# Kernel tuning notes

Hardware: AMD Instinct MI355X
Metric: run time of the kernel (lower is better)

## Reference

```python
import jax, jax.numpy as jnp
import numpy as np

B, NQ, NKV, D, H = 2, 2048, 2048, 1024, 16
DH = D // H
EPS = 1e-5


def _ln(x, g, b):
    mu = jnp.mean(x, axis=-1, keepdims=True)
    var = jnp.mean(jnp.square(x - mu), axis=-1, keepdims=True)
    return (x - mu) * jax.lax.rsqrt(var + EPS) * g + b


def setup_inputs() -> dict:
    key = jax.random.key(0)
    ks = jax.random.split(key, 16)
    s = 0.02
    return {
        "X": jax.random.normal(ks[0], (B, NQ, D), jnp.float32),
        "Y": jax.random.normal(ks[1], (B, NKV, D), jnp.float32),
        "Wq": jax.random.normal(ks[2], (D, D), jnp.float32) * s,
        "bq": jnp.zeros((D,), jnp.float32),
        "Wk": jax.random.normal(ks[3], (D, D), jnp.float32) * s,
        "bk": jnp.zeros((D,), jnp.float32),
        "Wv": jax.random.normal(ks[4], (D, D), jnp.float32) * s,
        "bv": jnp.zeros((D,), jnp.float32),
        "null_k": jax.random.normal(ks[5], (1, 1, D), jnp.float32) * s,
        "g0": jnp.ones((D,), jnp.float32),
        "b0": jnp.zeros((D,), jnp.float32),
        "g0kv": jnp.ones((D,), jnp.float32),
        "b0kv": jnp.zeros((D,), jnp.float32),
        "g1": jnp.ones((D,), jnp.float32),
        "b1": jnp.zeros((D,), jnp.float32),
        "W1": jax.random.normal(ks[6], (D, 4 * D), jnp.float32) * s,
        "bf1": jnp.zeros((4 * D,), jnp.float32),
        "W2": jax.random.normal(ks[7], (4 * D, D), jnp.float32) * s,
        "bf2": jnp.zeros((D,), jnp.float32),
    }


def reference(X, Y, Wq, bq, Wk, bk, Wv, bv, null_k, g0, b0, g0kv, b0kv,
              g1, b1, W1, bf1, W2, bf2):
    # pre-layer-norm on Q-side and KV-side inputs
    Xn = _ln(X, g0, b0)
    Yn = _ln(Y, g0kv, b0kv)
    Q = Xn @ Wq + bq                       # [B, NQ, D]
    K = Yn @ Wk + bk                       # [B, NKV, D]
    V = Yn @ Wv + bv
    # null KV: learned null key, zero value appended along seq dim
    K = jnp.concatenate([K, jnp.broadcast_to(null_k, (B, 1, D))], axis=1)   # [B, NKV+1, D]
    V = jnp.concatenate([V, jnp.zeros((B, 1, D), V.dtype)], axis=1)
    # split heads (split along feature dim == reshape to (.., H, DH))
    Qh = Q.reshape(B, NQ, H, DH)
    Kh = K.reshape(B, NKV + 1, H, DH)
    Vh = V.reshape(B, NKV + 1, H, DH)
    # scores scaled by 1/sqrt(dim_KV) (NOT head dim), softmax_temp == 1.0
    A = jnp.einsum('bqhd,bkhd->bhqk', Qh, Kh) / jnp.sqrt(jnp.float32(D))
    A = jax.nn.softmax(A, axis=-1)          # [B, H, NQ, NKV+1]
    O = jnp.einsum('bhqk,bkhd->bqhd', A, Vh).reshape(B, NQ, D)
    # no head mixing (fc_mix_heads=None); residual uses identity fc_res
    Hres = O + X
    Hr = _ln(Hres, g1, b1)
    ff = jax.nn.gelu(Hr @ W1 + bf1, approximate=False) @ W2 + bf2
    return Hres + ff
```

## Files before the change

### kernel.cpp

```cpp
#include <hip/hip_runtime.h>
#include <hip/hip_bf16.h>
#include <math.h>
#include <stdint.h>

typedef __bf16 bf16x8 __attribute__((ext_vector_type(8)));
typedef __bf16 bf16x4 __attribute__((ext_vector_type(4)));
typedef float floatx4 __attribute__((ext_vector_type(4)));
typedef short shortx4 __attribute__((ext_vector_type(4)));
typedef unsigned int uint32x2 __attribute__((ext_vector_type(2)));

#define NQS   2048
#define NKVS  2048
#define NKV1  2049
#define DM    1024
#define NH    16
#define DHD   64
#define BATCH 2
#define ROWS  (BATCH * NQS)

__device__ __forceinline__ void gld_lds16(const __bf16* gp, __bf16* lp) {
    __builtin_amdgcn_global_load_lds(
        (const __attribute__((address_space(1))) uint32_t*)(uintptr_t)gp,
        (__attribute__((address_space(3))) uint32_t*)(uintptr_t)lp,
        16, 0, 0);
}

__device__ __forceinline__ float gelu_fast(float x) {
    const float u = x * x;
    const float e = __builtin_amdgcn_exp2f(x * (-2.3022077f + (-0.1029431f) * u));
    return x * __builtin_amdgcn_rcpf(1.0f + e);
}

__global__ __launch_bounds__(256) void ln2_to_bf16(
    const float* __restrict__ X, const float* __restrict__ Y,
    const float* __restrict__ g0, const float* __restrict__ b0,
    const float* __restrict__ g0kv, const float* __restrict__ b0kv,
    __bf16* __restrict__ Xn, __bf16* __restrict__ Yn)
{
    int row = blockIdx.x;
    const float *src, *gamma, *beta; __bf16* dst;
    if (row < ROWS) { src = X; gamma = g0; beta = b0; dst = Xn; }
    else { row -= ROWS; src = Y; gamma = g0kv; beta = b0kv; dst = Yn; }
    const int tid = threadIdx.x;
    const float4 v = ((const float4*)(src + (size_t)row * DM))[tid];
    float s  = v.x + v.y + v.z + v.w;
    float sq = v.x * v.x + v.y * v.y + v.z * v.z + v.w * v.w;
    for (int off = 1; off < 64; off <<= 1) {
        s  += __shfl_xor(s, off);
        sq += __shfl_xor(sq, off);
    }
    __shared__ float red[8];
    const int wave = tid >> 6, lane = tid & 63;
    if (lane == 0) { red[wave * 2] = s; red[wave * 2 + 1] = sq; }
    __syncthreads();
    s  = red[0] + red[2] + red[4] + red[6];
    sq = red[1] + red[3] + red[5] + red[7];
    const float mu  = s * (1.0f / DM);
    const float var = sq * (1.0f / DM) - mu * mu;
    const float rs  = rsqrtf(var + 1e-5f);
    const float4 gv = ((const float4*)gamma)[tid];
    const float4 bv = ((const float4*)beta)[tid];
    bf16x4 o;
    o[0] = (__bf16)((v.x - mu) * rs * gv.x + bv.x);
    o[1] = (__bf16)((v.y - mu) * rs * gv.y + bv.y);
    o[2] = (__bf16)((v.z - mu) * rs * gv.z + bv.z);
    o[3] = (__bf16)((v.w - mu) * rs * gv.w + bv.w);
    *(bf16x4*)(dst + (size_t)row * DM + tid * 4) = o;
}

__global__ __launch_bounds__(256) void resid_ln(
    const float* __restrict__ X, const __bf16* __restrict__ O,
    const float* __restrict__ gamma, const float* __restrict__ beta,
    float* __restrict__ Hres, __bf16* __restrict__ Hr)
{
    const int row = blockIdx.x;
    const int tid = threadIdx.x;
    const float4 xv = ((const float4*)(X + (size_t)row * DM))[tid];
    const bf16x4 ov = *(const bf16x4*)(O + (size_t)row * DM + tid * 4);
    float4 v;
    v.x = xv.x + (float)ov[0];
    v.y = xv.y + (float)ov[1];
    v.z = xv.z + (float)ov[2];
    v.w = xv.w + (float)ov[3];
    ((float4*)(Hres + (size_t)row * DM))[tid] = v;

    float s  = v.x + v.y + v.z + v.w;
    float sq = v.x * v.x + v.y * v.y + v.z * v.z + v.w * v.w;
    for (int off = 1; off < 64; off <<= 1) {
        s  += __shfl_xor(s, off);
        sq += __shfl_xor(sq, off);
    }
    __shared__ float red[8];
    const int wave = tid >> 6, lane = tid & 63;
    if (lane == 0) { red[wave * 2] = s; red[wave * 2 + 1] = sq; }
    __syncthreads();
    s  = red[0] + red[2] + red[4] + red[6];
    sq = red[1] + red[3] + red[5] + red[7];
    const float mu  = s * (1.0f / DM);
    const float var = sq * (1.0f / DM) - mu * mu;
    const float rs  = rsqrtf(var + 1e-5f);
    const float4 gv = ((const float4*)gamma)[tid];
    const float4 bv = ((const float4*)beta)[tid];
    bf16x4 o;
    o[0] = (__bf16)((v.x - mu) * rs * gv.x + bv.x);
    o[1] = (__bf16)((v.y - mu) * rs * gv.y + bv.y);
    o[2] = (__bf16)((v.z - mu) * rs * gv.z + bv.z);
    o[3] = (__bf16)((v.w - mu) * rs * gv.w + bv.w);
    *(bf16x4*)(Hr + (size_t)row * DM + tid * 4) = o;
}

__global__ __launch_bounds__(256) void transpose3_f32_bf16(
    const float* __restrict__ Wq, const float* __restrict__ Wk,
    const float* __restrict__ Wv, __bf16* __restrict__ WqT,
    __bf16* __restrict__ WkT, __bf16* __restrict__ WvT)
{
    __shared__ float tile[32][33];
    const int z = blockIdx.z;
    const float* in = (z == 0) ? Wq : (z == 1) ? Wk : Wv;
    __bf16* out = (z == 0) ? WqT : (z == 1) ? WkT : WvT;
    const int c0 = blockIdx.x * 32, r0 = blockIdx.y * 32;
    const int tx = threadIdx.x, ty = threadIdx.y;
#pragma unroll
    for (int i = 0; i < 4; i++)
        tile[ty + i * 8][tx] = in[(size_t)(r0 + ty + i * 8) * DM + c0 + tx];
    __syncthreads();
#pragma unroll
    for (int i = 0; i < 4; i++)
        out[(size_t)(c0 + ty + i * 8) * DM + r0 + tx] = (__bf16)tile[tx][ty + i * 8];
}

__global__ __launch_bounds__(256) void transpose_ffw(
    const float* __restrict__ W1, const float* __restrict__ W2,
    __bf16* __restrict__ W1T, __bf16* __restrict__ W2T)
{
    __shared__ float tile[32][33];
    const int z = blockIdx.z;
    const float* in; __bf16* out; int R, C, c0, r0;
    if (z == 0) { in = W1; out = W1T; R = DM; C = 4 * DM; c0 = blockIdx.x * 32; r0 = blockIdx.y * 32; }
    else        { in = W2; out = W2T; R = 4 * DM; C = DM; c0 = blockIdx.y * 32; r0 = blockIdx.x * 32; }
    const int tx = threadIdx.x, ty = threadIdx.y;
#pragma unroll
    for (int i = 0; i < 4; i++)
        tile[ty + i * 8][tx] = in[(size_t)(r0 + ty + i * 8) * C + c0 + tx];
    __syncthreads();
#pragma unroll
    for (int i = 0; i < 4; i++)
        out[(size_t)(c0 + ty + i * 8) * R + r0 + tx] = (__bf16)tile[tx][ty + i * 8];
}

__global__ __launch_bounds__(256) void fill_null(
    const float* __restrict__ null_k, __bf16* __restrict__ Kb,
    __bf16* __restrict__ Vt)
{
    const int i = blockIdx.x * 256 + threadIdx.x;
    if (i < BATCH * DM) {
        const int b = i >> 10, d = i & (DM - 1);
        Kb[((size_t)b * NKV1 + NKVS) * DM + d] = (__bf16)null_k[d];
    }
    if (i < BATCH * NH * DHD * 8) {
        const int bhd = i >> 3, kvp = i & 7;
        Vt[(size_t)bhd * 2056 + 2048 + kvp] = (__bf16)0.0f;
    }
}

template<int MODE, int ACT>
__global__ __launch_bounds__(256) void gemm_bt(
    const __bf16* __restrict__ A, const __bf16* __restrict__ Bt,
    const float* __restrict__ bias, void* __restrict__ outp,
    const float* __restrict__ resid, int M, int N, int K)
{
    __shared__ __bf16 As[128][32];
    __shared__ __bf16 Bs[128][32];
    const int tid  = threadIdx.x;
    const int lane = tid & 63, wave = tid >> 6;
    const int g = lane >> 4, c = lane & 15;
    const int m0 = blockIdx.y * 128, n0 = blockIdx.x * 128;
    const int wm = (wave >> 1) * 64, wn = (wave & 1) * 64;

    floatx4 acc[4][4] = {};

    const int srow = tid >> 2;
    const int schk = (tid & 3) * 8;
    const __bf16* Ag = A  + (size_t)(m0 + srow) * K + schk;
    const __bf16* Bg = Bt + (size_t)(n0 + srow) * K + schk;
    __bf16* lA0 = &As[srow][schk];
    __bf16* lA1 = &As[srow + 64][schk];
    __bf16* lB0 = &Bs[srow][schk];
    __bf16* lB1 = &Bs[srow + 64][schk];

    int kbeg = 0, kend = K;
    if (MODE == 4) { const int KS = K >> 2; kbeg = blockIdx.z * KS; kend = kbeg + KS; }

    for (int k0 = kbeg; k0 < kend; k0 += 32) {
        __syncthreads();
        gld_lds16(Ag + k0, lA0);
        gld_lds16(Ag + (size_t)64 * K + k0, lA1);
        gld_lds16(Bg + k0, lB0);
        gld_lds16(Bg + (size_t)64 * K + k0, lB1);
        __syncthreads();
        bf16x8 af[4], bfr[4];
#pragma unroll
        for (int i = 0; i < 4; i++) af[i]  = *(const bf16x8*)&As[wm + i * 16 + c][g * 8];
#pragma unroll
        for (int j = 0; j < 4; j++) bfr[j] = *(const bf16x8*)&Bs[wn + j * 16 + c][g * 8];
#pragma unroll
        for (int i = 0; i < 4; i++)
#pragma unroll
            for (int j = 0; j < 4; j++)
                acc[i][j] = __builtin_amdgcn_mfma_f32_16x16x32_bf16(af[i], bfr[j], acc[i][j], 0, 0, 0);
    }

    __bf16* obf = (__bf16*)outp;
    float*  of  = (float*)outp;
#pragma unroll
    for (int i = 0; i < 4; i++) {
#pragma unroll
        for (int j = 0; j < 4; j++) {
            const int row = m0 + wm + i * 16 + g * 4;
            const int col = n0 + wn + j * 16 + c;
            const float bb = (MODE == 4) ? 0.0f : bias[col];
            float xs[4];
#pragma unroll
            for (int r = 0; r < 4; r++) {
                float x = acc[i][j][r] + bb;
                if (ACT == 1) x = gelu_fast(x);
                xs[r] = x;
            }
            if (MODE == 0) {
#pragma unroll
                for (int r = 0; r < 4; r++)
                    obf[(size_t)(row + r) * N + col] = (__bf16)xs[r];
            } else if (MODE == 4) {
#pragma unroll
                for (int r = 0; r < 4; r++)
                    of[((size_t)blockIdx.z * M + row + r) * N + col] = xs[r];
            }
        }
    }
}

__global__ __launch_bounds__(256) void qkv_gemm(
    const __bf16* __restrict__ Xn, const __bf16* __restrict__ Yn,
    const __bf16* __restrict__ WqT, const __bf16* __restrict__ WkT,
    const __bf16* __restrict__ WvT,
    const float* __restrict__ bq, const float* __restrict__ bk,
    const float* __restrict__ bv,
    __bf16* __restrict__ Qbf, __bf16* __restrict__ Kbf,
    __bf16* __restrict__ Vt)
{
    __shared__ __bf16 As[128][32];
    __shared__ __bf16 Bs[128][32];
    const int z = blockIdx.z;
    const __bf16* A    = (z == 0) ? Xn  : Yn;
    const __bf16* Bt   = (z == 0) ? WqT : (z == 1) ? WkT : WvT;
    const float*  bias = (z == 0) ? bq  : (z == 1) ? bk  : bv;

    const int tid  = threadIdx.x;
    const int lane = tid & 63, wave = tid >> 6;
    const int g = lane >> 4, c = lane & 15;
    const int m0 = blockIdx.y * 128, n0 = blockIdx.x * 128;
    const int wm = (wave >> 1) * 64, wn = (wave & 1) * 64;

    floatx4 acc[4][4] = {};

    const int srow = tid >> 2;
    const int schk = (tid & 3) * 8;
    const __bf16* Ag = A  + (size_t)(m0 + srow) * DM + schk;
    const __bf16* Bg = Bt + (size_t)(n0 + srow) * DM + schk;
    __bf16* lA0 = &As[srow][schk];
    __bf16* lA1 = &As[srow + 64][schk];
    __bf16* lB0 = &Bs[srow][schk];
    __bf16* lB1 = &Bs[srow + 64][schk];

    for (int k0 = 0; k0 < DM; k0 += 32) {
        __syncthreads();
        gld_lds16(Ag + k0, lA0);
        gld_lds16(Ag + (size_t)64 * DM + k0, lA1);
        gld_lds16(Bg + k0, lB0);
        gld_lds16(Bg + (size_t)64 * DM + k0, lB1);
        __syncthreads();
        bf16x8 af[4], bfr[4];
#pragma unroll
        for (int i = 0; i < 4; i++) af[i]  = *(const bf16x8*)&As[wm + i * 16 + c][g * 8];
#pragma unroll
        for (int j = 0; j < 4; j++) bfr[j] = *(const bf16x8*)&Bs[wn + j * 16 + c][g * 8];
#pragma unroll
        for (int i = 0; i < 4; i++)
#pragma unroll
            for (int j = 0; j < 4; j++)
                acc[i][j] = __builtin_amdgcn_mfma_f32_16x16x32_bf16(af[i], bfr[j], acc[i][j], 0, 0, 0);
    }

#pragma unroll
    for (int i = 0; i < 4; i++) {
#pragma unroll
        for (int j = 0; j < 4; j++) {
            const int row = m0 + wm + i * 16 + g * 4;
            const int col = n0 + wn + j * 16 + c;
            const float bb = bias[col];
            float xs[4];
#pragma unroll
            for (int r = 0; r < 4; r++) xs[r] = acc[i][j][r] + bb;
            if (z == 0) {
#pragma unroll
                for (int r = 0; r < 4; r++)
                    Qbf[(size_t)(row + r) * DM + col] = (__bf16)xs[r];
            } else if (z == 1) {
#pragma unroll
                for (int r = 0; r < 4; r++) {
                    const int rr = row + r;
                    Kbf[(size_t)(rr + (rr >> 11)) * DM + col] = (__bf16)xs[r];
                }
            } else {
                const int b  = row >> 11;
                const int kv = row & 2047;
                const size_t base =
                    ((size_t)((b * NH + (col >> 6)) * DHD + (col & 63))) * 2056 + kv;
                bf16x4 pk;
                pk[0] = (__bf16)xs[0]; pk[1] = (__bf16)xs[1];
                pk[2] = (__bf16)xs[2]; pk[3] = (__bf16)xs[3];
                *(bf16x4*)(Vt + base) = pk;
            }
        }
    }
}

__global__ __launch_bounds__(256) void ff2_reduce(
    const float* __restrict__ part, const float* __restrict__ bias,
    const float* __restrict__ Hres, float* __restrict__ out)
{
    const size_t f4 = (size_t)blockIdx.x * 256 + threadIdx.x;
    const int c4 = (int)(f4 & (DM / 4 - 1));
    const size_t stride4 = (size_t)ROWS * DM / 4;
    float4 a = ((const float4*)part)[f4];
    const float4 p1 = ((const float4*)part)[f4 + stride4];
    const float4 p2 = ((const float4*)part)[f4 + 2 * stride4];
    const float4 p3 = ((const float4*)part)[f4 + 3 * stride4];
    const float4 b  = ((const float4*)bias)[c4];
    const float4 hr = ((const float4*)Hres)[f4];
    a.x += p1.x + p2.x + p3.x + b.x + hr.x;
    a.y += p1.y + p2.y + p3.y + b.y + hr.y;
    a.z += p1.z + p2.z + p3.z + b.z + hr.z;
    a.w += p1.w + p2.w + p3.w + b.w + hr.w;
    ((float4*)out)[f4] = a;
}

__global__ __launch_bounds__(256, 2) void attn_kernel(
    const __bf16* __restrict__ Q, const __bf16* __restrict__ Kb,
    const __bf16* __restrict__ Vt, __bf16* __restrict__ O)
{
    __shared__ __bf16 Ks[2][64][64];
    __shared__ __bf16 Vs[2][64][64];

    const int tid = threadIdx.x, lane = tid & 63, w = tid >> 6;
    const int g = lane >> 4, c = lane & 15;

    const int hw   = blockIdx.x;
    const int slot = hw >> 3;
    const int hb   = (hw & 7) | ((slot >> 4) << 3);
    const int h = hb & 15, b = hb >> 4;
    const int q0w = (slot & 15) * 128 + w * 32;

    const float QSC = 0.03125f * 1.44269504088896f;
    bf16x8 qf[2][2];
#pragma unroll
    for (int qt = 0; qt < 2; qt++) {
        const __bf16* Qbase = Q + ((size_t)(b * NQS + q0w + qt * 16 + c)) * DM + h * DHD;
        qf[qt][0] = *(const bf16x8*)(Qbase + g * 8);
        qf[qt][1] = *(const bf16x8*)(Qbase + 32 + g * 8);
#pragma unroll
        for (int e = 0; e < 8; e++) {
            qf[qt][0][e] = (__bf16)((float)qf[qt][0][e] * QSC);
            qf[qt][1][e] = (__bf16)((float)qf[qt][1][e] * QSC);
        }
    }

    floatx4 lacc[2] = {};
    floatx4 oacc[2][4] = {};

    const int srow = tid >> 3;
    const int schk = (tid & 7) ^ (srow & 7);
    const __bf16* Kg  = Kb + (size_t)b * NKV1 * DM + h * DHD + schk * 8;
    const __bf16* Vg  = Vt + ((size_t)(b * NH + h) * DHD + srow) * 2056;
    const __bf16* Vg2 = Vg + (size_t)32 * 2056;
    const int vcol0 = schk * 8;

    auto stage = [&](int p, int kv0, bool tail) {
        __bf16* kd0 = &Ks[p][0][0]  + tid * 8;
        __bf16* kd1 = &Ks[p][32][0] + tid * 8;
        __bf16* vd0 = &Vs[p][0][0]  + tid * 8;
        __bf16* vd1 = &Vs[p][32][0] + tid * 8;
        if (!tail) {
            gld_lds16(Kg + (size_t)(kv0 + srow) * DM, kd0);
            gld_lds16(Kg + (size_t)(kv0 + srow + 32) * DM, kd1);
            gld_lds16(Vg + kv0 + vcol0, vd0);
            gld_lds16(Vg2 + kv0 + vcol0, vd1);
        } else {
            const int r0 = min(kv0 + srow, NKVS);
            const int r1 = min(kv0 + srow + 32, NKVS);
            const int vc = min(kv0 + vcol0, NKVS);
            gld_lds16(Kg + (size_t)r0 * DM, kd0);
            gld_lds16(Kg + (size_t)r1 * DM, kd1);
            gld_lds16(Vg + vc, vd0);
            gld_lds16(Vg2 + vc, vd1);
        }
    };

    auto compute = [&](int p, int kv0, bool tail) {
        floatx4 s[2][4];
#pragma unroll
        for (int qt = 0; qt < 2; qt++)
#pragma unroll
            for (int kvt = 0; kvt < 4; kvt++)
#pragma unroll
                for (int r = 0; r < 4; r++) s[qt][kvt][r] = -6.0f;

        const int sw = c & 7;
        __builtin_amdgcn_s_setprio(1);
#pragma unroll
        for (int kvt = 0; kvt < 4; kvt++) {
            const bf16x8 kf0 = *(const bf16x8*)&Ks[p][kvt * 16 + c][(g ^ sw) * 8];
            const bf16x8 kf1 = *(const bf16x8*)&Ks[p][kvt * 16 + c][((4 | g) ^ sw) * 8];
#pragma unroll
            for (int qt = 0; qt < 2; qt++) {
                s[qt][kvt] = __builtin_amdgcn_mfma_f32_16x16x32_bf16(kf0, qf[qt][0], s[qt][kvt], 0, 0, 0);
                s[qt][kvt] = __builtin_amdgcn_mfma_f32_16x16x32_bf16(kf1, qf[qt][1], s[qt][kvt], 0, 0, 0);
            }
        }
        __builtin_amdgcn_s_setprio(0);

        if (tail) {
#pragma unroll
            for (int qt = 0; qt < 2; qt++)
#pragma unroll
                for (int kvt = 0; kvt < 4; kvt++)
#pragma unroll
                    for (int r = 0; r < 4; r++)
                        if (kv0 + kvt * 16 + g * 4 + r >= NKV1) s[qt][kvt][r] = -1e30f;
        }

        shortx4 pf[2][4];
#pragma unroll
        for (int qt = 0; qt < 2; qt++)
#pragma unroll
            for (int kvt = 0; kvt < 4; kvt++) {
                float p0 = __builtin_amdgcn_exp2f(s[qt][kvt][0]);
                float p1 = __builtin_amdgcn_exp2f(s[qt][kvt][1]);
                float p2 = __builtin_amdgcn_exp2f(s[qt][kvt][2]);
                float p3 = __builtin_amdgcn_exp2f(s[qt][kvt][3]);
                lacc[qt][0] += p0; lacc[qt][1] += p1;
                lacc[qt][2] += p2; lacc[qt][3] += p3;
                uint32x2 pk;
                pk[0] = (__builtin_bit_cast(unsigned int, p0) >> 16) |
                        (__builtin_bit_cast(unsigned int, p1) & 0xFFFF0000u);
                pk[1] = (__builtin_bit_cast(unsigned int, p2) >> 16) |
                        (__builtin_bit_cast(unsigned int, p3) & 0xFFFF0000u);
                pf[qt][kvt] = __builtin_bit_cast(shortx4, pk);
            }

        __builtin_amdgcn_s_setprio(1);
#pragma unroll
        for (int kvt = 0; kvt < 4; kvt++) {
            shortx4 vfr[4];
#pragma unroll
            for (int dt = 0; dt < 4; dt++) {
                const int slotp = (kvt * 2 + (g >> 1)) ^ sw;
                vfr[dt] = *(const shortx4*)&Vs[p][dt * 16 + c][slotp * 8 + (g & 1) * 4];
            }
#pragma unroll
            for (int dt = 0; dt < 4; dt++)
#pragma unroll
                for (int qt = 0; qt < 2; qt++)
                    oacc[qt][dt] = __builtin_amdgcn_mfma_f32_16x16x16bf16_1k(
                        vfr[dt], pf[qt][kvt], oacc[qt][dt], 0, 0, 0);
        }
        __builtin_amdgcn_s_setprio(0);
    };

    stage(0, 0, false);
    __syncthreads();
    for (int it = 0; it < 32; it++) {
        stage((it + 1) & 1, (it + 1) * 64, it == 31);
        compute(it & 1, it * 64, false);
        __syncthreads();
    }
    compute(0, 2048, true);

#pragma unroll
    for (int qt = 0; qt < 2; qt++) {
        float l = lacc[qt][0] + lacc[qt][1] + lacc[qt][2] + lacc[qt][3];
        l += __shfl_xor(l, 16);
        l += __shfl_xor(l, 32);
        const float inv_l = 1.0f / l;
        __bf16* Ob = O + ((size_t)(b * NQS + q0w + qt * 16 + c)) * DM + h * DHD;
#pragma unroll
        for (int dt = 0; dt < 4; dt++) {
            bf16x4 ob;
#pragma unroll
            for (int r = 0; r < 4; r++) ob[r] = (__bf16)(oacc[qt][dt][r] * inv_l);
            *(bf16x4*)(Ob + dt * 16 + g * 4) = ob;
        }
    }
}

extern "C" void kernel_launch(void* const* d_in, const int* in_sizes, int n_in,
                              void* d_out, int out_size, void* d_ws, size_t ws_size,
                              hipStream_t stream)
{
    const float* X      = (const float*)d_in[0];
    const float* Y      = (const float*)d_in[1];
    const float* Wq     = (const float*)d_in[2];
    const float* bq     = (const float*)d_in[3];
    const float* Wk     = (const float*)d_in[4];
    const float* bk     = (const float*)d_in[5];
    const float* Wv     = (const float*)d_in[6];
    const float* bv     = (const float*)d_in[7];
    const float* null_k = (const float*)d_in[8];
    const float* g0     = (const float*)d_in[9];
    const float* b0     = (const float*)d_in[10];
    const float* g0kv   = (const float*)d_in[11];
    const float* b0kv   = (const float*)d_in[12];
    const float* g1     = (const float*)d_in[13];
    const float* b1     = (const float*)d_in[14];
    const float* W1     = (const float*)d_in[15];
    const float* bf1    = (const float*)d_in[16];
    const float* W2     = (const float*)d_in[17];
    const float* bf2    = (const float*)d_in[18];
    float* out = (float*)d_out;

    char* p = (char*)d_ws;
    __bf16* W2T  = (__bf16*)p; p += (size_t)4 * DM * DM * 2;
    float*  Hres = (float*)p;  p += (size_t)ROWS * DM * 4;
    __bf16* Gbf  = (__bf16*)p; p += (size_t)ROWS * 4 * DM * 2;
    char* scratch = p;
    __bf16* Xn   = (__bf16*)p; p += (size_t)ROWS * DM * 2;
    __bf16* Yn   = (__bf16*)p; p += (size_t)ROWS * DM * 2;
    __bf16* WqT  = (__bf16*)p; p += (size_t)DM * DM * 2;
    __bf16* WkT  = (__bf16*)p; p += (size_t)DM * DM * 2;
    __bf16* WvT  = (__bf16*)p; p += (size_t)DM * DM * 2;
    __bf16* W1T  = (__bf16*)p; p += (size_t)4 * DM * DM * 2;
    __bf16* Qbf  = (__bf16*)p; p += (size_t)ROWS * DM * 2;
    __bf16* Kbf  = (__bf16*)p; p += (size_t)BATCH * NKV1 * DM * 2;
    __bf16* Vt   = (__bf16*)p; p += (size_t)BATCH * NH * DHD * 2056 * 2;
    __bf16* Obf  = (__bf16*)p; p += (size_t)ROWS * DM * 2;
    __bf16* Hr   = (__bf16*)p; p += (size_t)ROWS * DM * 2;
    float* Part  = (float*)scratch;

    ln2_to_bf16<<<2 * ROWS, 256, 0, stream>>>(X, Y, g0, b0, g0kv, b0kv, Xn, Yn);

    transpose3_f32_bf16<<<dim3(DM / 32, DM / 32, 3), dim3(32, 8), 0, stream>>>(
        Wq, Wk, Wv, WqT, WkT, WvT);
    transpose_ffw<<<dim3(128, 32, 2), dim3(32, 8), 0, stream>>>(W1, W2, W1T, W2T);

    qkv_gemm<<<dim3(DM / 128, ROWS / 128, 3), 256, 0, stream>>>(
        Xn, Yn, WqT, WkT, WvT, bq, bk, bv, Qbf, Kbf, Vt);
    fill_null<<<64, 256, 0, stream>>>(null_k, Kbf, Vt);

    attn_kernel<<<dim3(512), 256, 0, stream>>>(Qbf, Kbf, Vt, Obf);

    resid_ln<<<ROWS, 256, 0, stream>>>(X, Obf, g1, b1, Hres, Hr);

    gemm_bt<0, 1><<<dim3(4 * DM / 128, ROWS / 128), 256, 0, stream>>>(
        Hr, W1T, bf1, (void*)Gbf, nullptr, ROWS, 4 * DM, DM);
    gemm_bt<4, 0><<<dim3(DM / 128, ROWS / 128, 4), 256, 0, stream>>>(
        Gbf, W2T, bf2, (void*)Part, nullptr, ROWS, DM, 4 * DM);
    ff2_reduce<<<ROWS * DM / 1024, 256, 0, stream>>>(Part, bf2, Hres, out);
}
```

Before: 390.1 us.

## Replace GEMMs with 256x256 tiles and four-stage async LDS pipeline

Replaces the 128x128 single-buffered GEMM kernels (QKV, FF1, FF2) with a shared 256x256-tile, 512-thread main loop. It keeps four LDS stages in flight using global_load_lds with explicit vmcnt waits, XOR-swizzles the LDS layout to avoid bank conflicts, raises wave priority around the MFMA block, and remaps block ids for L2 locality. The goal is to hide global load latency and raise MFMA utilization. In exchange it uses much more LDS (128KB per block) and fewer blocks, so occupancy drops and the tail is coarser, e.g. only 192 blocks for QKV.

```diff
diff --git a/kernel.cpp b/kernel.cpp
--- a/kernel.cpp
+++ b/kernel.cpp
@@ -163,83 +163,135 @@
     }
 }
 
-template<int MODE, int ACT>
-__global__ __launch_bounds__(256) void gemm_bt(
+__device__ __forceinline__ void g256_loop(
+    const __bf16* __restrict__ A, const __bf16* __restrict__ Bt,
+    int Kst, int kbeg, int m0, int n0,
+    __bf16* sa, __bf16* sb, floatx4 (&acc)[8][4])
+{
+    const int tid = threadIdx.x, lane = tid & 63;
+    const int g = lane >> 4, c = lane & 15;
+    const int wave = tid >> 6;
+    const int wm = wave >> 2, wn = wave & 3;
+
+    const int r = tid >> 2, j = tid & 3;
+    const int jx = (j ^ (r & 3)) * 8;
+    const __bf16* Ag = A  + (size_t)(m0 + r) * Kst + kbeg + jx;
+    const __bf16* Bg = Bt + (size_t)(n0 + r) * Kst + kbeg + jx;
+    __bf16* la = sa + tid * 8;
+    __bf16* lb = sb + tid * 8;
+
+#define G256_STAGE(ss, koff) do {                                          \
+    gld_lds16(Ag + (koff),                      la + (ss) * 8192);         \
+    gld_lds16(Ag + (size_t)128 * Kst + (koff),  la + (ss) * 8192 + 4096);  \
+    gld_lds16(Bg + (koff),                      lb + (ss) * 8192);         \
+    gld_lds16(Bg + (size_t)128 * Kst + (koff),  lb + (ss) * 8192 + 4096);  \
+} while (0)
+
+    G256_STAGE(0, 0);
+    G256_STAGE(1, 32);
+    G256_STAGE(2, 64);
+
+    const int ca = (c & 3) * 8;
+    const __bf16* ra = sa + (wm * 128 + c) * 32;
+    const __bf16* rb = sb + (wn * 64 + c) * 32;
+
+    for (int s = 0; s < 32; s++) {
+        if (s < 29) {
+            G256_STAGE((s + 3) & 3, (s + 3) * 32);
+            asm volatile("s_waitcnt vmcnt(12)" ::: "memory");
+        } else if (s == 29) {
+            asm volatile("s_waitcnt vmcnt(8)" ::: "memory");
+        } else if (s == 30) {
+            asm volatile("s_waitcnt vmcnt(4)" ::: "memory");
+        } else {
+            asm volatile("s_waitcnt vmcnt(0)" ::: "memory");
+        }
+        __builtin_amdgcn_sched_barrier(0);
+        __builtin_amdgcn_s_barrier();
+        asm volatile("" ::: "memory");
+
+        const int ss = (s & 3) * 8192;
+        bf16x8 af[8], bfr[4];
+#pragma unroll
+        for (int i = 0; i < 8; i++)
+            af[i] = *(const bf16x8*)(ra + ss + i * 512 + ((g * 8) ^ ca));
+#pragma unroll
+        for (int jj = 0; jj < 4; jj++)
+            bfr[jj] = *(const bf16x8*)(rb + ss + jj * 512 + ((g * 8) ^ ca));
+
+        __builtin_amdgcn_s_setprio(1);
+#pragma unroll
+        for (int i = 0; i < 8; i++)
+#pragma unroll
+            for (int jj = 0; jj < 4; jj++)
+                acc[i][jj] = __builtin_amdgcn_mfma_f32_16x16x32_bf16(
+                    af[i], bfr[jj], acc[i][jj], 0, 0, 0);
+        __builtin_amdgcn_s_setprio(0);
+        __builtin_amdgcn_sched_barrier(0);
+        __builtin_amdgcn_s_barrier();
+        asm volatile("" ::: "memory");
+    }
+#undef G256_STAGE
+}
+
+template<int NX>
+__device__ __forceinline__ void g256_decode(int bid, int ntot, int& m0, int& n0)
+{
+    const int cpx = ntot >> 3;
+    const int l = (bid & 7) * cpx + (bid >> 3);
+    m0 = (l / NX) * 256;
+    n0 = (l % NX) * 256;
+}
+
+template<int MODE, int ACT, int NX>
+__global__ __launch_bounds__(512, 2) void g256(
     const __bf16* __restrict__ A, const __bf16* __restrict__ Bt,
     const float* __restrict__ bias, void* __restrict__ outp,
-    const float* __restrict__ resid, int M, int N, int K)
-{
-    __shared__ __bf16 As[128][32];
-    __shared__ __bf16 Bs[128][32];
-    const int tid  = threadIdx.x;
-    const int lane = tid & 63, wave = tid >> 6;
+    int M, int N, int Kst)
+{
+    __shared__ __bf16 SA[4][256][32];
+    __shared__ __bf16 SB[4][256][32];
+    int m0, n0;
+    g256_decode<NX>(blockIdx.x, NX * (M >> 8), m0, n0);
+    const int kbeg = (MODE == 4) ? (blockIdx.z << 10) : 0;
+
+    floatx4 acc[8][4] = {};
+    g256_loop(A, Bt, Kst, kbeg, m0, n0, &SA[0][0][0], &SB[0][0][0], acc);
+
+    const int tid = threadIdx.x, lane = tid & 63, wave = tid >> 6;
     const int g = lane >> 4, c = lane & 15;
-    const int m0 = blockIdx.y * 128, n0 = blockIdx.x * 128;
-    const int wm = (wave >> 1) * 64, wn = (wave & 1) * 64;
-
-    floatx4 acc[4][4] = {};
-
-    const int srow = tid >> 2;
-    const int schk = (tid & 3) * 8;
-    const __bf16* Ag = A  + (size_t)(m0 + srow) * K + schk;
-    const __bf16* Bg = Bt + (size_t)(n0 + srow) * K + schk;
-    __bf16* lA0 = &As[srow][schk];
-    __bf16* lA1 = &As[srow + 64][schk];
-    __bf16* lB0 = &Bs[srow][schk];
-    __bf16* lB1 = &Bs[srow + 64][schk];
-
-    int kbeg = 0, kend = K;
-    if (MODE == 4) { const int KS = K >> 2; kbeg = blockIdx.z * KS; kend = kbeg + KS; }
-
-    for (int k0 = kbeg; k0 < kend; k0 += 32) {
-        __syncthreads();
-        gld_lds16(Ag + k0, lA0);
-        gld_lds16(Ag + (size_t)64 * K + k0, lA1);
-        gld_lds16(Bg + k0, lB0);
-        gld_lds16(Bg + (size_t)64 * K + k0, lB1);
-        __syncthreads();
-        bf16x8 af[4], bfr[4];
-#pragma unroll
-        for (int i = 0; i < 4; i++) af[i]  = *(const bf16x8*)&As[wm + i * 16 + c][g * 8];
-#pragma unroll
-        for (int j = 0; j < 4; j++) bfr[j] = *(const bf16x8*)&Bs[wn + j * 16 + c][g * 8];
-#pragma unroll
-        for (int i = 0; i < 4; i++)
-#pragma unroll
-            for (int j = 0; j < 4; j++)
-                acc[i][j] = __builtin_amdgcn_mfma_f32_16x16x32_bf16(af[i], bfr[j], acc[i][j], 0, 0, 0);
-    }
+    const int wm = wave >> 2, wn = wave & 3;
 
     __bf16* obf = (__bf16*)outp;
     float*  of  = (float*)outp;
 #pragma unroll
-    for (int i = 0; i < 4; i++) {
-#pragma unroll
-        for (int j = 0; j < 4; j++) {
-            const int row = m0 + wm + i * 16 + g * 4;
-            const int col = n0 + wn + j * 16 + c;
+    for (int i = 0; i < 8; i++) {
+#pragma unroll
+        for (int jj = 0; jj < 4; jj++) {
+            const int row = m0 + wm * 128 + i * 16 + g * 4;
+            const int col = n0 + wn * 64 + jj * 16 + c;
             const float bb = (MODE == 4) ? 0.0f : bias[col];
             float xs[4];
 #pragma unroll
-            for (int r = 0; r < 4; r++) {
-                float x = acc[i][j][r] + bb;
+            for (int rr = 0; rr < 4; rr++) {
+                float x = acc[i][jj][rr] + bb;
                 if (ACT == 1) x = gelu_fast(x);
-                xs[r] = x;
+                xs[rr] = x;
             }
             if (MODE == 0) {
 #pragma unroll
-                for (int r = 0; r < 4; r++)
-                    obf[(size_t)(row + r) * N + col] = (__bf16)xs[r];
+                for (int rr = 0; rr < 4; rr++)
+                    obf[(size_t)(row + rr) * N + col] = (__bf16)xs[rr];
             } else if (MODE == 4) {
 #pragma unroll
-                for (int r = 0; r < 4; r++)
-                    of[((size_t)blockIdx.z * M + row + r) * N + col] = xs[r];
+                for (int rr = 0; rr < 4; rr++)
+                    of[((size_t)blockIdx.z * M + row + rr) * N + col] = xs[rr];
             }
         }
     }
 }
 
-__global__ __launch_bounds__(256) void qkv_gemm(
+__global__ __launch_bounds__(512, 2) void g256qkv(
     const __bf16* __restrict__ Xn, const __bf16* __restrict__ Yn,
     const __bf16* __restrict__ WqT, const __bf16* __restrict__ WkT,
     const __bf16* __restrict__ WvT,
@@ -248,68 +300,42 @@
     __bf16* __restrict__ Qbf, __bf16* __restrict__ Kbf,
     __bf16* __restrict__ Vt)
 {
-    __shared__ __bf16 As[128][32];
-    __shared__ __bf16 Bs[128][32];
+    __shared__ __bf16 SA[4][256][32];
+    __shared__ __bf16 SB[4][256][32];
     const int z = blockIdx.z;
     const __bf16* A    = (z == 0) ? Xn  : Yn;
     const __bf16* Bt   = (z == 0) ? WqT : (z == 1) ? WkT : WvT;
     const float*  bias = (z == 0) ? bq  : (z == 1) ? bk  : bv;
 
-    const int tid  = threadIdx.x;
-    const int lane = tid & 63, wave = tid >> 6;
+    int m0, n0;
+    g256_decode<4>(blockIdx.x, 64, m0, n0);
+
+    floatx4 acc[8][4] = {};
+    g256_loop(A, Bt, DM, 0, m0, n0, &SA[0][0][0], &SB[0][0][0], acc);
+
+    const int tid = threadIdx.x, lane = tid & 63, wave = tid >> 6;
     const int g = lane >> 4, c = lane & 15;
-    const int m0 = blockIdx.y * 128, n0 = blockIdx.x * 128;
-    const int wm = (wave >> 1) * 64, wn = (wave & 1) * 64;
-
-    floatx4 acc[4][4] = {};
-
-    const int srow = tid >> 2;
-    const int schk = (tid & 3) * 8;
-    const __bf16* Ag = A  + (size_t)(m0 + srow) * DM + schk;
-    const __bf16* Bg = Bt + (size_t)(n0 + srow) * DM + schk;
-    __bf16* lA0 = &As[srow][schk];
-    __bf16* lA1 = &As[srow + 64][schk];
-    __bf16* lB0 = &Bs[srow][schk];
-    __bf16* lB1 = &Bs[srow + 64][schk];
-
-    for (int k0 = 0; k0 < DM; k0 += 32) {
-        __syncthreads();
-        gld_lds16(Ag + k0, lA0);
-        gld_lds16(Ag + (size_t)64 * DM + k0, lA1);
-        gld_lds16(Bg + k0, lB0);
-        gld_lds16(Bg + (size_t)64 * DM + k0, lB1);
-        __syncthreads();
-        bf16x8 af[4], bfr[4];
-#pragma unroll
-        for (int i = 0; i < 4; i++) af[i]  = *(const bf16x8*)&As[wm + i * 16 + c][g * 8];
-#pragma unroll
-        for (int j = 0; j < 4; j++) bfr[j] = *(const bf16x8*)&Bs[wn + j * 16 + c][g * 8];
-#pragma unroll
-        for (int i = 0; i < 4; i++)
-#pragma unroll
-            for (int j = 0; j < 4; j++)
-                acc[i][j] = __builtin_amdgcn_mfma_f32_16x16x32_bf16(af[i], bfr[j], acc[i][j], 0, 0, 0);
-    }
-
-#pragma unroll
-    for (int i = 0; i < 4; i++) {
-#pragma unroll
-        for (int j = 0; j < 4; j++) {
-            const int row = m0 + wm + i * 16 + g * 4;
-            const int col = n0 + wn + j * 16 + c;
+    const int wm = wave >> 2, wn = wave & 3;
+
+#pragma unroll
+    for (int i = 0; i < 8; i++) {
+#pragma unroll
+        for (int jj = 0; jj < 4; jj++) {
+            const int row = m0 + wm * 128 + i * 16 + g * 4;
+            const int col = n0 + wn * 64 + jj * 16 + c;
             const float bb = bias[col];
             float xs[4];
 #pragma unroll
-            for (int r = 0; r < 4; r++) xs[r] = acc[i][j][r] + bb;
+            for (int rr = 0; rr < 4; rr++) xs[rr] = acc[i][jj][rr] + bb;
             if (z == 0) {
 #pragma unroll
-                for (int r = 0; r < 4; r++)
-                    Qbf[(size_t)(row + r) * DM + col] = (__bf16)xs[r];
+                for (int rr = 0; rr < 4; rr++)
+                    Qbf[(size_t)(row + rr) * DM + col] = (__bf16)xs[rr];
             } else if (z == 1) {
 #pragma unroll
-                for (int r = 0; r < 4; r++) {
-                    const int rr = row + r;
-                    Kbf[(size_t)(rr + (rr >> 11)) * DM + col] = (__bf16)xs[r];
+                for (int rr = 0; rr < 4; rr++) {
+                    const int r2 = row + rr;
+                    Kbf[(size_t)(r2 + (r2 >> 11)) * DM + col] = (__bf16)xs[rr];
                 }
             } else {
                 const int b  = row >> 11;
@@ -552,7 +578,7 @@
         Wq, Wk, Wv, WqT, WkT, WvT);
     transpose_ffw<<<dim3(128, 32, 2), dim3(32, 8), 0, stream>>>(W1, W2, W1T, W2T);
 
-    qkv_gemm<<<dim3(DM / 128, ROWS / 128, 3), 256, 0, stream>>>(
+    g256qkv<<<dim3(64, 1, 3), 512, 0, stream>>>(
         Xn, Yn, WqT, WkT, WvT, bq, bk, bv, Qbf, Kbf, Vt);
     fill_null<<<64, 256, 0, stream>>>(null_k, Kbf, Vt);
 
@@ -560,9 +586,9 @@
 
     resid_ln<<<ROWS, 256, 0, stream>>>(X, Obf, g1, b1, Hres, Hr);
 
-    gemm_bt<0, 1><<<dim3(4 * DM / 128, ROWS / 128), 256, 0, stream>>>(
-        Hr, W1T, bf1, (void*)Gbf, nullptr, ROWS, 4 * DM, DM);
-    gemm_bt<4, 0><<<dim3(DM / 128, ROWS / 128, 4), 256, 0, stream>>>(
-        Gbf, W2T, bf2, (void*)Part, nullptr, ROWS, DM, 4 * DM);
+    g256<0, 1, 16><<<dim3(256), 512, 0, stream>>>(
+        Hr, W1T, bf1, (void*)Gbf, ROWS, 4 * DM, DM);
+    g256<4, 0, 4><<<dim3(64, 1, 4), 512, 0, stream>>>(
+        Gbf, W2T, bf2, (void*)Part, ROWS, DM, 4 * DM);
     ff2_reduce<<<ROWS * DM / 1024, 256, 0, stream>>>(Part, bf2, Hres, out);
 }
```

Result: faster. 349.1 us (-10.5%).
